# Performance work log

Hardware: AMD Instinct MI355X
Metric: run time of the kernel (lower is better)

Reference implementation:

```python
import jax, jax.numpy as jnp
import numpy as np

HIDDEN = 2048
HEADS = 16
HEAD_DIM = HIDDEN // HEADS
ROPE_THETA = 10000.0


def setup_inputs() -> dict:
    key = jax.random.key(0)
    ks = jax.random.split(key, 5)
    B, S = 2, 2048
    hidden_states = jax.random.normal(ks[0], (B, S, HIDDEN), dtype=jnp.float32)
    position_ids = jnp.broadcast_to(jnp.arange(S, dtype=jnp.int64), (B, S))
    # Linear params (torch Linear: y = x @ W.T + b); store as [in, out]
    sc = 1.0 / np.sqrt(HIDDEN)
    Wqkv = jax.random.uniform(ks[1], (HIDDEN, 3 * HIDDEN), jnp.float32, -sc, sc)
    bqkv = jax.random.uniform(ks[2], (3 * HIDDEN,), jnp.float32, -sc, sc)
    Wo = jax.random.uniform(ks[3], (HIDDEN, HIDDEN), jnp.float32, -sc, sc)
    bo = jax.random.uniform(ks[4], (HIDDEN,), jnp.float32, -sc, sc)
    return {"hidden_states": hidden_states, "position_ids": position_ids,
            "Wqkv": Wqkv, "bqkv": bqkv, "Wo": Wo, "bo": bo}


def _rotate_half(x):
    x1, x2 = jnp.split(x, 2, axis=-1)
    return jnp.concatenate([-x2, x1], axis=-1)


def _rope_cos_sin(position_ids):
    # inv_freq: [Dh/2]
    inv_freq = 1.0 / (ROPE_THETA ** (jnp.arange(0, HEAD_DIM, 2, dtype=jnp.float32) / HEAD_DIM))
    ang = position_ids.astype(jnp.float32)[..., None] * inv_freq  # [B,S,Dh/2]
    emb = jnp.concatenate([ang, ang], axis=-1)  # [B,S,Dh]
    return jnp.cos(emb)[:, None], jnp.sin(emb)[:, None]  # [B,1,S,Dh]


def reference(hidden_states, position_ids, Wqkv, bqkv, Wo, bo):
    B, S, _ = hidden_states.shape
    qkv = hidden_states @ Wqkv + bqkv  # [B,S,3*H*Dh]
    qkv = qkv.reshape(B, S, 3, HEADS, HEAD_DIM).transpose(2, 0, 3, 1, 4)
    q, k, v = qkv[0], qkv[1], qkv[2]  # each [B,H,S,Dh]
    cos, sin = _rope_cos_sin(position_ids)
    q = q * cos + _rotate_half(q) * sin
    k = k * cos + _rotate_half(k) * sin
    scale = HEAD_DIM ** -0.5
    scores = jnp.einsum('bhqd,bhkd->bhqk', q, k) * scale
    mask = jnp.triu(jnp.full((S, S), -jnp.inf, dtype=scores.dtype), k=1)
    attn = jax.nn.softmax(scores + mask, axis=-1)
    out = jnp.einsum('bhqk,bhkd->bhqd', attn, v)
    out = out.transpose(0, 2, 1, 3).reshape(B, S, HIDDEN)
    return out @ Wo + bo
```

## Files before the change

### kernel.cpp

```cpp
#include <hip/hip_runtime.h>
#include <stdint.h>

typedef __attribute__((ext_vector_type(8))) short bf16x8;
typedef __attribute__((ext_vector_type(4))) float f32x4;

__device__ __forceinline__ float bf2f(ushort u) {
  union { uint32_t u; float f; } v; v.u = ((uint32_t)u) << 16; return v.f;
}
__device__ __forceinline__ ushort f2bf(float f) {
  union { float f; uint32_t u; } v; v.f = f;
  uint32_t r = (v.u + 0x7fffu + ((v.u >> 16) & 1u)) >> 16;
  return (ushort)r;
}

__device__ __forceinline__ f32x4 mfma16(bf16x8 a, bf16x8 b, f32x4 c) {
  return __builtin_amdgcn_mfma_f32_16x16x32_bf16(a, b, c, 0, 0, 0);
}

__device__ __forceinline__ void glds16(const ushort* g, ushort* l) {
  __builtin_amdgcn_global_load_lds(
      (__attribute__((address_space(1))) void*)(void*)g,
      (__attribute__((address_space(3))) void*)(void*)l, 16, 0, 0);
}

#define BAR()  __builtin_amdgcn_s_barrier()
#define LGK0() asm volatile("s_waitcnt lgkmcnt(0)" ::: "memory")
#define LGK8() asm volatile("s_waitcnt lgkmcnt(8)" ::: "memory")
#define VMC4() asm volatile("s_waitcnt vmcnt(4)" ::: "memory")
#define VMC6() asm volatile("s_waitcnt vmcnt(6)" ::: "memory")
#define VMC0() asm volatile("s_waitcnt vmcnt(0)" ::: "memory")
#define SCB0() __builtin_amdgcn_sched_barrier(0)
#define PRIO1() __builtin_amdgcn_s_setprio(1)
#define PRIO0() __builtin_amdgcn_s_setprio(0)

__global__ __launch_bounds__(256) void cast_f32_bf16(
    const float* __restrict__ in, ushort* __restrict__ out, long n) {
  const long i = ((long)blockIdx.x * 256 + threadIdx.x) * 4;
  if (i + 3 >= n) {
    for (long j = i; j < n; j++) out[j] = f2bf(in[j]);
    return;
  }
  const float4 v = *(const float4*)&in[i];
  ushort4 o;
  o.x = f2bf(v.x); o.y = f2bf(v.y); o.z = f2bf(v.z); o.w = f2bf(v.w);
  *(ushort4*)&out[i] = o;
}

__global__ __launch_bounds__(256) void transpose_cast(
    const float* __restrict__ in, ushort* __restrict__ out, int R, int C) {
  __shared__ ushort t[32][33];
  const int tx = threadIdx.x & 31, ty = threadIdx.x >> 5;
  const int bc = blockIdx.x * 32;
  const int br = blockIdx.y * 32;
#pragma unroll
  for (int i = 0; i < 32; i += 8)
    t[ty + i][tx] = f2bf(in[(long)(br + ty + i) * C + bc + tx]);
  __syncthreads();
#pragma unroll
  for (int i = 0; i < 32; i += 8)
    out[(long)(bc + ty + i) * R + br + tx] = t[tx][ty + i];
}


__device__ __forceinline__ void stg2(const ushort* src, ushort* dst, long kstride) {
  glds16(src, dst);
  glds16(src + 64 * kstride, dst + 4096);
}

__device__ __forceinline__ void rd4(bf16x8 (&d)[4][2], const ushort* p,
                                    int kq0, int kq1) {
#pragma unroll
  for (int ii = 0; ii < 4; ii++) {
    d[ii][0] = *(const bf16x8*)&p[ii * 1024 + kq0];
    d[ii][1] = *(const bf16x8*)&p[ii * 1024 + kq1];
  }
}
__device__ __forceinline__ void rd2(bf16x8 (&d)[2][2], const ushort* p,
                                    int kq0, int kq1) {
#pragma unroll
  for (int jj = 0; jj < 2; jj++) {
    d[jj][0] = *(const bf16x8*)&p[jj * 1024 + kq0];
    d[jj][1] = *(const bf16x8*)&p[jj * 1024 + kq1];
  }
}
template <int I0, int J0>
__device__ __forceinline__ void mmq(f32x4 (&acc)[8][4], const bf16x8 (&a)[4][2],
                                    const bf16x8 (&b)[2][2]) {
#pragma unroll
  for (int ii = 0; ii < 4; ii++)
#pragma unroll
    for (int jj = 0; jj < 2; jj++)
#pragma unroll
      for (int ks = 0; ks < 2; ks++)
        acc[I0 + ii][J0 + jj] =
            mfma16(a[ii][ks], b[jj][ks], acc[I0 + ii][J0 + jj]);
}

template <bool F32OUT>
__global__ __launch_bounds__(512, 2) void gemm256(
    const ushort* __restrict__ A, const ushort* __restrict__ Bt,
    const float* __restrict__ bias, void* __restrict__ Cout,
    int N, int K, int NBM) {
  __shared__ ushort lds[2][2][16384];
  const int tid = threadIdx.x;
  const int wave = tid >> 6, lane = tid & 63;
  const int quad = lane >> 4, l16 = lane & 15;
  const int wm = wave >> 2, wn = wave & 3;
  const long Kl = K;

  const int nwg = gridDim.x;
  const int wg = ((int)blockIdx.x & 7) * (nwg >> 3) + ((int)blockIdx.x >> 3);
  const int bm = (wg % NBM) * 256;
  const int bn = (wg / NBM) * 256;
  const int NT = K >> 6;

  const int srow = (wave << 3) + (lane >> 3);
  const int kc8 = ((lane & 7) ^ ((lane >> 3) & 7)) << 3;
  const ushort* Asrc = A + (long)(bm + srow) * Kl + kc8;
  const ushort* Bsrc = Bt + (long)(bn + srow) * Kl + kc8;

#define STAGE(SRC, BUF, MAT, H, KT)                                       \
  stg2(SRC + (long)(H) * 128 * Kl + (long)(KT) * 64,                      \
       &lds[BUF][MAT][(H) * 8192 + (wave << 9)], Kl)

  const int kq0 = (quad ^ (l16 & 7)) << 3;
  const int kq1 = ((4 | quad) ^ (l16 & 7)) << 3;

  f32x4 acc[8][4] = {};

  STAGE(Bsrc, 0, 1, 0, 0); STAGE(Bsrc, 0, 1, 1, 0);
  STAGE(Asrc, 0, 0, 0, 0); STAGE(Asrc, 0, 0, 1, 0);
  STAGE(Bsrc, 1, 1, 0, 1); STAGE(Bsrc, 1, 1, 1, 1);
  STAGE(Asrc, 1, 0, 0, 1);
  VMC6(); BAR();

  const int NI = NT >> 1;
#pragma unroll 1
  for (int t = 0; t < NI; ++t) {
    const int kb  = 2 * t + 1;
    const int kp0 = (2 * t + 2 < NT) ? 2 * t + 2 : NT - 1;
    const int kp1 = (2 * t + 3 < NT) ? 2 * t + 3 : NT - 1;
    bf16x8 a[4][2], b0[2][2], b1[2][2];

    rd4(a, &lds[0][0][(wm * 128 + l16) * 64], kq0, kq1);
    rd2(b0, &lds[0][1][(wn * 64 + l16) * 64], kq0, kq1);
    STAGE(Asrc, 1, 0, 1, kb);
    LGK8();
    BAR(); LGK0(); SCB0();
    PRIO1(); mmq<0, 0>(acc, a, b0); PRIO0();
    BAR();

    rd2(b1, &lds[0][1][(wn * 64 + 32 + l16) * 64], kq0, kq1);
    BAR(); LGK0(); SCB0();
    PRIO1(); mmq<0, 2>(acc, a, b1); PRIO0();
    BAR();

    rd4(a, &lds[0][0][(wm * 128 + 64 + l16) * 64], kq0, kq1);
    STAGE(Bsrc, 0, 1, 0, kp0);
    BAR(); LGK0(); SCB0();
    PRIO1(); mmq<4, 0>(acc, a, b0); PRIO0();
    BAR();

    STAGE(Bsrc, 0, 1, 1, kp0);
    VMC4();
    BAR();
    PRIO1(); mmq<4, 2>(acc, a, b1); PRIO0();
    BAR();

    rd4(a, &lds[1][0][(wm * 128 + l16) * 64], kq0, kq1);
    rd2(b0, &lds[1][1][(wn * 64 + l16) * 64], kq0, kq1);
    STAGE(Asrc, 0, 0, 0, kp0);
    LGK8();
    BAR(); LGK0(); SCB0();
    PRIO1(); mmq<0, 0>(acc, a, b0); PRIO0();
    BAR();

    rd2(b1, &lds[1][1][(wn * 64 + 32 + l16) * 64], kq0, kq1);
    STAGE(Asrc, 0, 0, 1, kp0);
    BAR(); LGK0(); SCB0();
    PRIO1(); mmq<0, 2>(acc, a, b1); PRIO0();
    BAR();

    rd4(a, &lds[1][0][(wm * 128 + 64 + l16) * 64], kq0, kq1);
    STAGE(Bsrc, 1, 1, 0, kp1);
    BAR(); LGK0(); SCB0();
    PRIO1(); mmq<4, 0>(acc, a, b0); PRIO0();
    BAR();

    STAGE(Bsrc, 1, 1, 1, kp1);
    STAGE(Asrc, 1, 0, 0, kp1);
    VMC6();
    BAR();
    PRIO1(); mmq<4, 2>(acc, a, b1); PRIO0();
    BAR();
  }
  VMC0();

#pragma unroll
  for (int i = 0; i < 8; i++) {
#pragma unroll
    for (int j = 0; j < 4; j++) {
      const int col = bn + wn * 64 + j * 16 + l16;
      const float bv = bias[col];
#pragma unroll
      for (int r = 0; r < 4; r++) {
        const int row = bm + wm * 128 + i * 16 + quad * 4 + r;
        const float v = acc[i][j][r] + bv;
        if (F32OUT)
          ((float*)Cout)[(long)row * N + col] = v;
        else
          ((ushort*)Cout)[(long)row * N + col] = f2bf(v);
      }
    }
  }
#undef STAGE
}

__global__ __launch_bounds__(256) void rope_table(float* __restrict__ tab) {
  const int i = blockIdx.x * 256 + threadIdx.x;
  const int d = i & 63, s = i >> 6;
  const float f = powf(10000.0f, -(float)(2 * d) / 128.0f);
  const float ang = (float)s * f;
  tab[i] = cosf(ang);
  tab[131072 + i] = sinf(ang);
}

__global__ __launch_bounds__(256) void rope_apply(ushort* __restrict__ qkv,
                                                  const float* __restrict__ tab) {
  const int i = blockIdx.x * 256 + threadIdx.x;
  const int d8 = (i & 7) * 8;
  const int h = (i >> 3) & 15;
  const long bs = i >> 7;
  const int s = (int)(bs & 2047);
  const float* ct = &tab[(s << 6) + d8];
  const float* st = &tab[131072 + (s << 6) + d8];
  float c[8], sn[8];
  *(float4*)&c[0] = *(const float4*)&ct[0];
  *(float4*)&c[4] = *(const float4*)&ct[4];
  *(float4*)&sn[0] = *(const float4*)&st[0];
  *(float4*)&sn[4] = *(const float4*)&st[4];
  ushort* row = qkv + bs * 6144 + h * 128 + d8;
#pragma unroll
  for (int qk = 0; qk < 2; qk++) {
    ushort* p = row + qk * 2048;
    ushort x1[8] __attribute__((aligned(16)));
    ushort x2[8] __attribute__((aligned(16)));
    *(uint4*)x1 = *(const uint4*)p;
    *(uint4*)x2 = *(const uint4*)(p + 64);
#pragma unroll
    for (int e = 0; e < 8; e++) {
      const float a = bf2f(x1[e]), b2 = bf2f(x2[e]);
      x1[e] = f2bf(a * c[e] - b2 * sn[e]);
      x2[e] = f2bf(b2 * c[e] + a * sn[e]);
    }
    *(uint4*)p = *(uint4*)x1;
    *(uint4*)(p + 64) = *(uint4*)x2;
  }
}

#define KSTR 136
#define VSTR 68
__global__ __launch_bounds__(256) void attn_part(
    const ushort* __restrict__ qkv, float* __restrict__ part_o,
    float* __restrict__ part_l, int T, int slots_bh) {
  const int S = 2048, LD = 6144;
  const int tid = threadIdx.x;
  const int wave = tid >> 6, lane = tid & 63;
  const int quad = lane >> 4, l16 = lane & 15;
  const int h = blockIdx.y;
  const int b = blockIdx.z;

  int y = blockIdx.x, qt = -1, ch = 0;
  for (int q = 31; q >= 0; --q) {
    const int c = q / T + 1;
    if (qt < 0) {
      if (y < c) { qt = q; ch = y; } else y -= c;
    }
  }
  int sb = 0;
  for (int q = 0; q < qt; q++) sb += q / T + 1;
  const long slot = ((long)(b * 16 + h)) * slots_bh + sb + ch;

  const ushort* base = qkv + (long)b * S * LD;
  const int qrow0 = qt * 64 + wave * 16;
  const int kb0 = ch * T * 64;
  const int kbend = min((ch + 1) * T * 64, qt * 64 + 64);

  __shared__ ushort Ks[64 * KSTR];
  __shared__ ushort Vs[128 * VSTR];
  __shared__ ushort Ps[4][16 * VSTR];

  bf16x8 qf[4];
  {
    const ushort* qp = base + (long)(qrow0 + l16) * LD + h * 128 + quad * 8;
#pragma unroll
    for (int c = 0; c < 4; c++) qf[c] = *(const bf16x8*)(qp + c * 32);
  }

  float l_lane[4] = {0.f, 0.f, 0.f, 0.f};
  f32x4 o[8];
#pragma unroll
  for (int f = 0; f < 8; f++) o[f] = (f32x4){0.f, 0.f, 0.f, 0.f};

  const float scale = 0.08838834764831845f;

  const int k_row = tid >> 4;
  const int k_dcol = (tid & 15) * 8;
  const int v_key2 = (tid & 31) * 2;
  const int v_dc0 = tid >> 5;

  for (int kb = kb0; kb < kbend; kb += 64) {
    __syncthreads();
#pragma unroll
    for (int it = 0; it < 4; it++) {
      const int row = k_row + it * 16;
      *(uint4*)&Ks[row * KSTR + k_dcol] =
          *(const uint4*)(base + (long)(kb + row) * LD + 2048 + h * 128 + k_dcol);
    }
#pragma unroll
    for (int it = 0; it < 2; it++) {
      const int dc = v_dc0 + it * 8;
      const ushort* vg = base + (long)(kb + v_key2) * LD + 4096 + h * 128 + dc * 8;
      ushort va[8] __attribute__((aligned(16)));
      ushort vb[8] __attribute__((aligned(16)));
      *(uint4*)va = *(const uint4*)vg;
      *(uint4*)vb = *(const uint4*)(vg + LD);
#pragma unroll
      for (int e = 0; e < 8; e++) {
        const uint32_t pk = (uint32_t)va[e] | ((uint32_t)vb[e] << 16);
        *(uint32_t*)&Vs[(dc * 8 + e) * VSTR + v_key2] = pk;
      }
    }
    __syncthreads();

    int nkt = (qrow0 + 15 - kb) / 16 + 1;
    if (nkt > 4) nkt = 4;

    f32x4 sc[4] = {};
#pragma unroll
    for (int kt = 0; kt < 4; kt++) {
      if (kt < nkt) {
#pragma unroll
        for (int c = 0; c < 4; c++) {
          bf16x8 kf = *(const bf16x8*)&Ks[(kt * 16 + l16) * KSTR + c * 32 + quad * 8];
          sc[kt] = mfma16(qf[c], kf, sc[kt]);
        }
      }
    }

#pragma unroll
    for (int r = 0; r < 4; r++) {
      const int qpos = qrow0 + quad * 4 + r;
      const int prow = (quad * 4 + r) * VSTR;
      float psum = 0.f;
#pragma unroll
      for (int kt = 0; kt < 4; kt++) {
        const float e = __expf(sc[kt][r] * scale);
        const float p = (kb + kt * 16 + l16 > qpos) ? 0.f : e;
        psum += p;
        Ps[wave][prow + kt * 16 + l16] = f2bf(p);
      }
      l_lane[r] += psum;
    }

    bf16x8 pf0 = *(const bf16x8*)&Ps[wave][l16 * VSTR + quad * 8];
#pragma unroll
    for (int f = 0; f < 8; f++) {
      bf16x8 vf0 = *(const bf16x8*)&Vs[(f * 16 + l16) * VSTR + quad * 8];
      o[f] = mfma16(pf0, vf0, o[f]);
    }
    if (nkt > 2) {
      bf16x8 pf1 = *(const bf16x8*)&Ps[wave][l16 * VSTR + 32 + quad * 8];
#pragma unroll
      for (int f = 0; f < 8; f++) {
        bf16x8 vf1 = *(const bf16x8*)&Vs[(f * 16 + l16) * VSTR + 32 + quad * 8];
        o[f] = mfma16(pf1, vf1, o[f]);
      }
    }
  }

  float* po = part_o + slot * 8192;
#pragma unroll
  for (int r = 0; r < 4; r++) {
    float l = l_lane[r];
    l += __shfl_xor(l, 1);
    l += __shfl_xor(l, 2);
    l += __shfl_xor(l, 4);
    l += __shfl_xor(l, 8);
    const int row = wave * 16 + quad * 4 + r;
#pragma unroll
    for (int f = 0; f < 8; f++)
      po[row * 128 + f * 16 + l16] = o[f][r];
    if (l16 == 0) part_l[slot * 64 + row] = l;
  }
}

__global__ __launch_bounds__(256) void attn_merge(
    const float* __restrict__ part_o, const float* __restrict__ part_l,
    ushort* __restrict__ attnb, int T, int slots_bh) {
  const int qt = blockIdx.x, h = blockIdx.y, b = blockIdx.z;
  const int tid = threadIdx.x;
  const int cnt = qt / T + 1;
  int sb = 0;
  for (int q = 0; q < qt; q++) sb += q / T + 1;
  const long slot0 = ((long)(b * 16 + h)) * slots_bh + sb;

  for (int e4 = tid; e4 < 2048; e4 += 256) {
    const int elem = e4 * 4;
    const int row = elem >> 7;
    const int d = elem & 127;
    float4 s = {0.f, 0.f, 0.f, 0.f};
    float l = 0.f;
    for (int c = 0; c < cnt; c++) {
      const float4 p = *(const float4*)&part_o[(slot0 + c) * 8192 + elem];
      s.x += p.x; s.y += p.y; s.z += p.z; s.w += p.w;
      l += part_l[(slot0 + c) * 64 + row];
    }
    const float inv = 1.0f / l;
    ushort4 ov;
    ov.x = f2bf(s.x * inv); ov.y = f2bf(s.y * inv);
    ov.z = f2bf(s.z * inv); ov.w = f2bf(s.w * inv);
    *(ushort4*)&attnb[((long)b * 2048 + qt * 64 + row) * 2048 + h * 128 + d] = ov;
  }
}

static const void* find_by_size(void* const* d_in, const int* in_sizes,
                                int n_in, long want) {
  for (int i = 0; i < n_in; i++)
    if ((long)in_sizes[i] == want) return d_in[i];
  return nullptr;
}

extern "C" void kernel_launch(void* const* d_in, const int* in_sizes, int n_in,
                              void* d_out, int out_size, void* d_ws, size_t ws_size,
                              hipStream_t stream) {
  const float* hidden = (const float*)find_by_size(d_in, in_sizes, n_in, 8388608);
  const float* Wqkv   = (const float*)find_by_size(d_in, in_sizes, n_in, 12582912);
  const float* bqkv   = (const float*)find_by_size(d_in, in_sizes, n_in, 6144);
  const float* Wo     = (const float*)find_by_size(d_in, in_sizes, n_in, 4194304);
  const float* bo     = (const float*)find_by_size(d_in, in_sizes, n_in, 2048);

  uintptr_t w = (uintptr_t)d_ws;
  ushort* hiddenB = (ushort*)w; w += (size_t)4096 * 2048 * 2;
  ushort* WqkvT   = (ushort*)w; w += (size_t)6144 * 2048 * 2;
  ushort* WoT     = (ushort*)w; w += (size_t)2048 * 2048 * 2;
  ushort* qkvb    = (ushort*)w; w += (size_t)4096 * 6144 * 2;
  ushort* attnb   = (ushort*)w; w += (size_t)4096 * 2048 * 2;
  float*  tab     = (float*)w;  w += (size_t)2048 * 64 * 2 * 4;
  const size_t fixed_bytes = w - (uintptr_t)d_ws;

  int T = 8, slots_bh = 0;
  for (;; T *= 2) {
    slots_bh = 0;
    for (int q = 0; q < 32; q++) slots_bh += q / T + 1;
    const size_t need = fixed_bytes +
        (size_t)slots_bh * 32 * (8192 + 64) * 4;
    if (need <= ws_size || T >= 32) break;
  }
  float* part_o = (float*)w; w += (size_t)slots_bh * 32 * 8192 * 4;
  float* part_l = (float*)w; w += (size_t)slots_bh * 32 * 64 * 4;

  cast_f32_bf16<<<8192, 256, 0, stream>>>(hidden, hiddenB, 8388608L);
  transpose_cast<<<dim3(192, 64), 256, 0, stream>>>(Wqkv, WqkvT, 2048, 6144);
  transpose_cast<<<dim3(64, 64), 256, 0, stream>>>(Wo, WoT, 2048, 2048);
  rope_table<<<512, 256, 0, stream>>>(tab);
  gemm256<false><<<dim3(384), 512, 0, stream>>>(hiddenB, WqkvT, bqkv,
                                                qkvb, 6144, 2048, 16);
  rope_apply<<<2048, 256, 0, stream>>>(qkvb, tab);
  attn_part<<<dim3(slots_bh, 16, 2), 256, 0, stream>>>(qkvb, part_o, part_l,
                                                       T, slots_bh);
  attn_merge<<<dim3(32, 16, 2), 256, 0, stream>>>(part_o, part_l, attnb,
                                                  T, slots_bh);
  gemm256<true><<<dim3(128), 512, 0, stream>>>(attnb, WoT, bo,
                                               d_out, 2048, 2048, 16);
}
```

Before: 443.9 us.

## Reschedule GEMM staging with fewer barriers; register-prefetch K/V in attention

```diff
diff --git a/kernel.cpp b/kernel.cpp
--- a/kernel.cpp
+++ b/kernel.cpp
@@ -26,8 +26,8 @@
 #define BAR()  __builtin_amdgcn_s_barrier()
 #define LGK0() asm volatile("s_waitcnt lgkmcnt(0)" ::: "memory")
 #define LGK8() asm volatile("s_waitcnt lgkmcnt(8)" ::: "memory")
+#define VMC2() asm volatile("s_waitcnt vmcnt(2)" ::: "memory")
 #define VMC4() asm volatile("s_waitcnt vmcnt(4)" ::: "memory")
-#define VMC6() asm volatile("s_waitcnt vmcnt(6)" ::: "memory")
 #define VMC0() asm volatile("s_waitcnt vmcnt(0)" ::: "memory")
 #define SCB0() __builtin_amdgcn_sched_barrier(0)
 #define PRIO1() __builtin_amdgcn_s_setprio(1)
@@ -131,8 +131,7 @@
   STAGE(Bsrc, 0, 1, 0, 0); STAGE(Bsrc, 0, 1, 1, 0);
   STAGE(Asrc, 0, 0, 0, 0); STAGE(Asrc, 0, 0, 1, 0);
   STAGE(Bsrc, 1, 1, 0, 1); STAGE(Bsrc, 1, 1, 1, 1);
-  STAGE(Asrc, 1, 0, 0, 1);
-  VMC6(); BAR();
+  VMC4(); BAR();
 
   const int NI = NT >> 1;
 #pragma unroll 1
@@ -144,55 +143,47 @@
 
     rd4(a, &lds[0][0][(wm * 128 + l16) * 64], kq0, kq1);
     rd2(b0, &lds[0][1][(wn * 64 + l16) * 64], kq0, kq1);
+    STAGE(Asrc, 1, 0, 0, kb);
     STAGE(Asrc, 1, 0, 1, kb);
     LGK8();
     BAR(); LGK0(); SCB0();
     PRIO1(); mmq<0, 0>(acc, a, b0); PRIO0();
+
+    rd2(b1, &lds[0][1][(wn * 64 + 32 + l16) * 64], kq0, kq1);
+    BAR(); LGK0(); SCB0();
+    PRIO1(); mmq<0, 2>(acc, a, b1); PRIO0();
+
+    rd4(a, &lds[0][0][(wm * 128 + 64 + l16) * 64], kq0, kq1);
+    BAR(); LGK0(); SCB0();
+    PRIO1(); mmq<4, 0>(acc, a, b0); PRIO0();
+
+    STAGE(Bsrc, 0, 1, 0, kp0);
+    VMC2();
     BAR();
-
-    rd2(b1, &lds[0][1][(wn * 64 + 32 + l16) * 64], kq0, kq1);
+    PRIO1(); mmq<4, 2>(acc, a, b1); PRIO0();
+
+    rd4(a, &lds[1][0][(wm * 128 + l16) * 64], kq0, kq1);
+    rd2(b0, &lds[1][1][(wn * 64 + l16) * 64], kq0, kq1);
+    STAGE(Bsrc, 0, 1, 1, kp0);
+    LGK8();
+    BAR(); LGK0(); SCB0();
+    PRIO1(); mmq<0, 0>(acc, a, b0); PRIO0();
+
+    rd2(b1, &lds[1][1][(wn * 64 + 32 + l16) * 64], kq0, kq1);
+    STAGE(Asrc, 0, 0, 0, kp0);
     BAR(); LGK0(); SCB0();
     PRIO1(); mmq<0, 2>(acc, a, b1); PRIO0();
-    BAR();
-
-    rd4(a, &lds[0][0][(wm * 128 + 64 + l16) * 64], kq0, kq1);
-    STAGE(Bsrc, 0, 1, 0, kp0);
+
+    rd4(a, &lds[1][0][(wm * 128 + 64 + l16) * 64], kq0, kq1);
+    STAGE(Asrc, 0, 0, 1, kp0);
     BAR(); LGK0(); SCB0();
     PRIO1(); mmq<4, 0>(acc, a, b0); PRIO0();
-    BAR();
-
-    STAGE(Bsrc, 0, 1, 1, kp0);
+
+    STAGE(Bsrc, 1, 1, 0, kp1);
+    STAGE(Bsrc, 1, 1, 1, kp1);
     VMC4();
     BAR();
     PRIO1(); mmq<4, 2>(acc, a, b1); PRIO0();
-    BAR();
-
-    rd4(a, &lds[1][0][(wm * 128 + l16) * 64], kq0, kq1);
-    rd2(b0, &lds[1][1][(wn * 64 + l16) * 64], kq0, kq1);
-    STAGE(Asrc, 0, 0, 0, kp0);
-    LGK8();
-    BAR(); LGK0(); SCB0();
-    PRIO1(); mmq<0, 0>(acc, a, b0); PRIO0();
-    BAR();
-
-    rd2(b1, &lds[1][1][(wn * 64 + 32 + l16) * 64], kq0, kq1);
-    STAGE(Asrc, 0, 0, 1, kp0);
-    BAR(); LGK0(); SCB0();
-    PRIO1(); mmq<0, 2>(acc, a, b1); PRIO0();
-    BAR();
-
-    rd4(a, &lds[1][0][(wm * 128 + 64 + l16) * 64], kq0, kq1);
-    STAGE(Bsrc, 1, 1, 0, kp1);
-    BAR(); LGK0(); SCB0();
-    PRIO1(); mmq<4, 0>(acc, a, b0); PRIO0();
-    BAR();
-
-    STAGE(Bsrc, 1, 1, 1, kp1);
-    STAGE(Asrc, 1, 0, 0, kp1);
-    VMC6();
-    BAR();
-    PRIO1(); mmq<4, 2>(acc, a, b1); PRIO0();
-    BAR();
   }
   VMC0();
 
@@ -309,22 +300,33 @@
   const int v_key2 = (tid & 31) * 2;
   const int v_dc0 = tid >> 5;
 
+  uint4 krg[4], vrg0[2], vrg1[2];
+  {
+    const ushort* kp = base + (long)(kb0 + k_row) * LD + 2048 + h * 128 + k_dcol;
+#pragma unroll
+    for (int it = 0; it < 4; it++)
+      krg[it] = *(const uint4*)(kp + (long)(it * 16) * LD);
+#pragma unroll
+    for (int it = 0; it < 2; it++) {
+      const ushort* vg =
+          base + (long)(kb0 + v_key2) * LD + 4096 + h * 128 + (v_dc0 + it * 8) * 8;
+      vrg0[it] = *(const uint4*)vg;
+      vrg1[it] = *(const uint4*)(vg + LD);
+    }
+  }
+
   for (int kb = kb0; kb < kbend; kb += 64) {
     __syncthreads();
 #pragma unroll
-    for (int it = 0; it < 4; it++) {
-      const int row = k_row + it * 16;
-      *(uint4*)&Ks[row * KSTR + k_dcol] =
-          *(const uint4*)(base + (long)(kb + row) * LD + 2048 + h * 128 + k_dcol);
-    }
+    for (int it = 0; it < 4; it++)
+      *(uint4*)&Ks[(k_row + it * 16) * KSTR + k_dcol] = krg[it];
 #pragma unroll
     for (int it = 0; it < 2; it++) {
       const int dc = v_dc0 + it * 8;
-      const ushort* vg = base + (long)(kb + v_key2) * LD + 4096 + h * 128 + dc * 8;
       ushort va[8] __attribute__((aligned(16)));
       ushort vb[8] __attribute__((aligned(16)));
-      *(uint4*)va = *(const uint4*)vg;
-      *(uint4*)vb = *(const uint4*)(vg + LD);
+      *(uint4*)va = vrg0[it];
+      *(uint4*)vb = vrg1[it];
 #pragma unroll
       for (int e = 0; e < 8; e++) {
         const uint32_t pk = (uint32_t)va[e] | ((uint32_t)vb[e] << 16);
@@ -332,6 +334,21 @@
       }
     }
     __syncthreads();
+
+    if (kb + 64 < kbend) {
+      const int kn = kb + 64;
+      const ushort* kp = base + (long)(kn + k_row) * LD + 2048 + h * 128 + k_dcol;
+#pragma unroll
+      for (int it = 0; it < 4; it++)
+        krg[it] = *(const uint4*)(kp + (long)(it * 16) * LD);
+#pragma unroll
+      for (int it = 0; it < 2; it++) {
+        const ushort* vg =
+            base + (long)(kn + v_key2) * LD + 4096 + h * 128 + (v_dc0 + it * 8) * 8;
+        vrg0[it] = *(const uint4*)vg;
+        vrg1[it] = *(const uint4*)(vg + LD);
+      }
+    }
 
     int nkt = (qrow0 + 15 - kb) / 16 + 1;
     if (nkt > 4) nkt = 4;
```

After: 481.0 us. 1.08x slower.
